# Optimization experiments

Measured on AMD Instinct MI355X. Metric: run time of the kernel, lower is better.

## Reference

```python
import jax, jax.numpy as jnp
import numpy as np

N = 50000      # nodes
E = 800000     # edges (before self loops)
F_IN = 128     # input feature dim
H = 4          # attention heads
C = 64         # per-head channels (hidden_dim = out_channels = 64)
HC = H * C     # 256, concat output width of each GATv2Conv
G = 32         # number of graphs in the batch
NEG_SLOPE_ATT = 0.2   # GATv2 internal LeakyReLU
NEG_SLOPE_ACT = 0.01  # encoder nn.LeakyReLU() default


def _glorot(key, shape, fan_in):
    return jax.random.normal(key, shape, jnp.float32) * (1.0 / np.sqrt(fan_in))


def setup_inputs() -> dict:
    key = jax.random.key(0)
    ks = jax.random.split(key, 32)
    inp = {}
    inp["x"] = jax.random.normal(ks[0], (N, F_IN), jnp.float32)
    inp["edge_index"] = jax.random.randint(ks[1], (2, E), 0, N, jnp.int32)
    inp["batch"] = jnp.sort(jax.random.randint(ks[2], (N,), 0, G, jnp.int32))
    i = 3
    for li, fin in ((1, F_IN), (2, HC), (3, HC)):
        inp[f"Wl{li}"] = _glorot(ks[i], (HC, fin), fin); i += 1
        inp[f"bl{li}"] = jnp.zeros((HC,), jnp.float32)
        inp[f"Wr{li}"] = _glorot(ks[i], (HC, fin), fin); i += 1
        inp[f"br{li}"] = jnp.zeros((HC,), jnp.float32)
        inp[f"att{li}"] = _glorot(ks[i], (H, C), C); i += 1
        inp[f"bo{li}"] = jnp.zeros((HC,), jnp.float32)
    return inp


def _gatv2_layer(x, src, dst, Wl, bl, Wr, br, att, bo):
    n = x.shape[0]
    xl = (x @ Wl.T + bl).reshape(n, H, C)  # source transform
    xr = (x @ Wr.T + br).reshape(n, H, C)  # target transform
    # per-edge attention logits: a^T LeakyReLU(xl[j] + xr[i])
    e = jax.nn.leaky_relu(xl[src] + xr[dst], negative_slope=NEG_SLOPE_ATT)  # [E', H, C]
    score = jnp.einsum('ehc,hc->eh', e, att)                                # [E', H]
    # segment softmax over incoming edges of each destination node
    m = jax.ops.segment_max(score, dst, num_segments=n)
    p = jnp.exp(score - m[dst])
    s = jax.ops.segment_sum(p, dst, num_segments=n)
    alpha = p / s[dst]
    out = jax.ops.segment_sum(alpha[:, :, None] * xl[src], dst, num_segments=n)
    return out.reshape(n, HC) + bo


def reference(x, edge_index, batch,
              Wl1, bl1, Wr1, br1, att1, bo1,
              Wl2, bl2, Wr2, br2, att2, bo2,
              Wl3, bl3, Wr3, br3, att3, bo3):
    loop = jnp.arange(N, dtype=edge_index.dtype)
    src = jnp.concatenate([edge_index[0], loop])  # add self loops (PyG default)
    dst = jnp.concatenate([edge_index[1], loop])
    h = _gatv2_layer(x, src, dst, Wl1, bl1, Wr1, br1, att1, bo1)
    h = jax.nn.leaky_relu(h, negative_slope=NEG_SLOPE_ACT)
    h = _gatv2_layer(h, src, dst, Wl2, bl2, Wr2, br2, att2, bo2)
    h = jax.nn.leaky_relu(h, negative_slope=NEG_SLOPE_ACT)
    h = _gatv2_layer(h, src, dst, Wl3, bl3, Wr3, br3, att3, bo3)
    # global mean pool over graphs
    sums = jax.ops.segment_sum(h, batch, num_segments=G)
    cnt = jax.ops.segment_sum(jnp.ones((N,), h.dtype), batch, num_segments=G)
    return sums / jnp.maximum(cnt, 1.0)[:, None]
```

## Files before the change

kernel.cpp:

```cpp
#include <hip/hip_runtime.h>

#define HEADS 4
#define CH 64
#define HC 256
#define NGRAPH 32
#define NEG_ATT 0.2f
#define NEG_ACT 0.01f

typedef __attribute__((ext_vector_type(8))) short bf16x8;
typedef __attribute__((ext_vector_type(4))) float f32x4;
typedef __attribute__((ext_vector_type(2))) float f32x2;

typedef __attribute__((address_space(3))) unsigned int lds_u32;
typedef const __attribute__((address_space(1))) unsigned int glob_u32;

__device__ __forceinline__ void gl_lds16(const void* g, void* l) {
  __builtin_amdgcn_global_load_lds((glob_u32*)(uintptr_t)g,
                                   (lds_u32*)(unsigned int)(uintptr_t)l, 16, 0, 0);
}

__device__ __forceinline__ void split2(float a, float b, unsigned& hi, unsigned& lo) {
  unsigned ua = __float_as_uint(a), ub = __float_as_uint(b);
  float la = a - __uint_as_float(ua & 0xFFFF0000u);
  float lb = b - __uint_as_float(ub & 0xFFFF0000u);
  hi = __builtin_amdgcn_perm(ub, ua, 0x07060302u);
  lo = __builtin_amdgcn_perm(__float_as_uint(lb), __float_as_uint(la), 0x07060302u);
}

__device__ __forceinline__ unsigned rtn_bf16(float f) {
  unsigned u = __float_as_uint(f);
  return (u + 0x7FFFu + ((u >> 16) & 1u)) >> 16;
}
__device__ __forceinline__ unsigned rtn_pack2(float a, float b) {
  return (rtn_bf16(b) << 16) | rtn_bf16(a);
}

__global__ __launch_bounds__(256) void convert_x(
    const float* __restrict__ X, unsigned short* __restrict__ xhi,
    unsigned short* __restrict__ xlo, int total4) {
  int g = blockIdx.x * 256 + threadIdx.x;
  if (g >= total4) return;
  float4 v = *(const float4*)&X[(size_t)g * 4];
  uint2 h2, l2;
  split2(v.x, v.y, h2.x, l2.x);
  split2(v.z, v.w, h2.y, l2.y);
  *(uint2*)&xhi[(size_t)g * 4] = h2;
  *(uint2*)&xlo[(size_t)g * 4] = l2;
}

__device__ __forceinline__ void conv_w_one(
    int g, const float* Wl, const float* Wr, int K,
    unsigned short* wfhi, unsigned short* wflo) {
  int lane = g & 63;
  int ct = (g >> 6) & 31;
  int kb = g >> 11;
  int col = ct * 16 + (lane & 15);
  int k = kb * 32 + (lane >> 4) * 8;
  const float* src = (col < HC) ? &Wl[(size_t)col * K + k] : &Wr[(size_t)(col - HC) * K + k];
  float4 v0 = *(const float4*)src;
  float4 v1 = *(const float4*)(src + 4);
  uint4 hq, lq;
  split2(v0.x, v0.y, hq.x, lq.x);
  split2(v0.z, v0.w, hq.y, lq.y);
  split2(v1.x, v1.y, hq.z, lq.z);
  split2(v1.z, v1.w, hq.w, lq.w);
  *(uint4*)&wfhi[(size_t)g * 8] = hq;
  *(uint4*)&wflo[(size_t)g * 8] = lq;
}

__global__ __launch_bounds__(256) void convert_w_all(
    const float* __restrict__ Wl1, const float* __restrict__ Wr1,
    unsigned short* __restrict__ w1hi, unsigned short* __restrict__ w1lo,
    const float* __restrict__ Wl2, const float* __restrict__ Wr2,
    unsigned short* __restrict__ w2hi, unsigned short* __restrict__ w2lo,
    const float* __restrict__ Wl3, const float* __restrict__ Wr3,
    unsigned short* __restrict__ w3hi, unsigned short* __restrict__ w3lo) {
  int g = blockIdx.x * 256 + threadIdx.x;
  if (g < 8192) conv_w_one(g, Wl1, Wr1, 128, w1hi, w1lo);
  else if (g < 8192 + 16384) conv_w_one(g - 8192, Wl2, Wr2, 256, w2hi, w2lo);
  else conv_w_one(g - 8192 - 16384, Wl3, Wr3, 256, w3hi, w3lo);
}

template <int K>
__global__ __launch_bounds__(256) void gemm_fused(
    const unsigned short* __restrict__ xhi, const unsigned short* __restrict__ xlo,
    const unsigned short* __restrict__ wfhi, const unsigned short* __restrict__ wflo,
    const float* __restrict__ bl, const float* __restrict__ br,
    unsigned short* __restrict__ Y1, unsigned short* __restrict__ Y2, int N, int nrb) {
  constexpr int nkb = K >> 5;
  __shared__ unsigned short Ah[2][128][32];
  __shared__ unsigned short Al[2][128][32];

  const int f = blockIdx.x;
  const int rb = (f & 7) + 8 * (f >> 5);
  const int cb = (f >> 3) & 3;
  if (rb >= nrb) return;

  const int tid = threadIdx.x;
  const int wave = tid >> 6;
  const int lane = tid & 63;
  const int quad = lane >> 4;
  const int l16 = lane & 15;
  const int wr = (wave >> 1) * 64;
  const int wc = (wave & 1) * 64;
  const int row0 = rb * 128;
  const int col0 = cb * 128;
  const int ctg0 = cb * 8 + (wave & 1) * 4;

  const int c0 = tid, c1 = tid + 256;
  const int r0g = row0 + (c0 >> 2), r1g = row0 + (c1 >> 2);
  const int ko0 = (c0 & 3) * 8, ko1 = (c1 & 3) * 8;
  const int gr0 = (r0g < N) ? r0g : N - 1;
  const int gr1 = (r1g < N) ? r1g : N - 1;

  f32x4 acc[4][4];
#pragma unroll
  for (int i = 0; i < 4; i++)
#pragma unroll
    for (int j = 0; j < 4; j++) acc[i][j] = (f32x4){0.f, 0.f, 0.f, 0.f};

  {
    size_t ga0 = (size_t)gr0 * K + ko0;
    size_t ga1 = (size_t)gr1 * K + ko1;
    gl_lds16(&xhi[ga0], &Ah[0][c0 >> 2][ko0]);
    gl_lds16(&xlo[ga0], &Al[0][c0 >> 2][ko0]);
    gl_lds16(&xhi[ga1], &Ah[0][c1 >> 2][ko1]);
    gl_lds16(&xlo[ga1], &Al[0][c1 >> 2][ko1]);
  }

#pragma unroll
  for (int kb = 0; kb < nkb; kb++) {
    const int cur = kb & 1, nxt = cur ^ 1;
    bf16x8 bhi[4], blo[4];
#pragma unroll
    for (int j = 0; j < 4; j++) {
      size_t ci = ((size_t)kb * 32 + ctg0 + j) * 64 + lane;
      bhi[j] = *(const bf16x8*)&wfhi[ci * 8];
      blo[j] = *(const bf16x8*)&wflo[ci * 8];
    }
    __syncthreads();
    if (kb + 1 < nkb) {
      int k0 = (kb + 1) * 32;
      size_t ga0 = (size_t)gr0 * K + k0 + ko0;
      size_t ga1 = (size_t)gr1 * K + k0 + ko1;
      gl_lds16(&xhi[ga0], &Ah[nxt][c0 >> 2][ko0]);
      gl_lds16(&xlo[ga0], &Al[nxt][c0 >> 2][ko0]);
      gl_lds16(&xhi[ga1], &Ah[nxt][c1 >> 2][ko1]);
      gl_lds16(&xlo[ga1], &Al[nxt][c1 >> 2][ko1]);
    }
    bf16x8 ahi[4], alo[4];
#pragma unroll
    for (int i = 0; i < 4; i++) {
      ahi[i] = *(const bf16x8*)&Ah[cur][wr + i * 16 + l16][quad * 8];
      alo[i] = *(const bf16x8*)&Al[cur][wr + i * 16 + l16][quad * 8];
    }
#pragma unroll
    for (int i = 0; i < 4; i++)
#pragma unroll
      for (int j = 0; j < 4; j++) {
        acc[i][j] = __builtin_amdgcn_mfma_f32_16x16x32_bf16(ahi[i], bhi[j], acc[i][j], 0, 0, 0);
        acc[i][j] = __builtin_amdgcn_mfma_f32_16x16x32_bf16(ahi[i], blo[j], acc[i][j], 0, 0, 0);
        acc[i][j] = __builtin_amdgcn_mfma_f32_16x16x32_bf16(alo[i], bhi[j], acc[i][j], 0, 0, 0);
      }
  }

#pragma unroll
  for (int j = 0; j < 4; j++) {
    int colg = col0 + wc + j * 16 + l16;
    unsigned short* Yp = (colg < HC) ? Y1 : Y2;
    int cc = (colg < HC) ? colg : colg - HC;
    float bv = (colg < HC) ? bl[cc] : br[cc];
#pragma unroll
    for (int i = 0; i < 4; i++)
#pragma unroll
      for (int r = 0; r < 4; r++) {
        int row = row0 + wr + i * 16 + quad * 4 + r;
        if (row < N)
          Yp[(size_t)row * HC + cc] = (unsigned short)rtn_bf16(acc[i][j][r] + bv);
      }
  }
}

__global__ __launch_bounds__(256) void hist_dst(
    const int* __restrict__ edst, int* __restrict__ counts, int E) {
  int e = blockIdx.x * 256 + threadIdx.x;
  if (e < E) atomicAdd(&counts[edst[e]], 1);
}

__global__ __launch_bounds__(256) void scan_blocks(
    const int* __restrict__ counts, int* __restrict__ row_start,
    int* __restrict__ bsum, int N) {
  __shared__ int tmp[256];
  int t = threadIdx.x;
  int base = blockIdx.x * 1024 + t * 4;
  int v0 = (base     < N) ? counts[base]     + 1 : 0;
  int v1 = (base + 1 < N) ? counts[base + 1] + 1 : 0;
  int v2 = (base + 2 < N) ? counts[base + 2] + 1 : 0;
  int v3 = (base + 3 < N) ? counts[base + 3] + 1 : 0;
  int c1 = v0 + v1, c2 = c1 + v2, tot = c2 + v3;
  tmp[t] = tot;
  __syncthreads();
  for (int off = 1; off < 256; off <<= 1) {
    int add = (t >= off) ? tmp[t - off] : 0;
    __syncthreads();
    tmp[t] += add;
    __syncthreads();
  }
  int excl = tmp[t] - tot;
  if (base     < N) row_start[base + 1] = excl + v0;
  if (base + 1 < N) row_start[base + 2] = excl + c1;
  if (base + 2 < N) row_start[base + 3] = excl + c2;
  if (base + 3 < N) row_start[base + 4] = excl + tot;
  if (t == 255) bsum[blockIdx.x] = tmp[255];
  if (blockIdx.x == 0 && t == 0) row_start[0] = 0;
}

__global__ void scan_tops(int* __restrict__ bsum, int nb) {
  int lane = threadIdx.x;
  int v = (lane < nb) ? bsum[lane] : 0;
  for (int off = 1; off < 64; off <<= 1) {
    int u = __shfl_up(v, off);
    if (lane >= off) v += u;
  }
  if (lane < nb) bsum[lane] = v;
}

__global__ __launch_bounds__(256) void scan_add(
    int* __restrict__ row_start, const int* __restrict__ bsum, int N) {
  int off = bsum[blockIdx.x];
  int i = (blockIdx.x + 1) * 1024 + threadIdx.x * 4;
#pragma unroll
  for (int k = 0; k < 4; k++)
    if (i + k < N) row_start[i + k + 1] += off;
}

__global__ __launch_bounds__(256) void csr_init(
    const int* __restrict__ row_start, int* __restrict__ fill_pos,
    int* __restrict__ csr_src, int N) {
  int i = blockIdx.x * 256 + threadIdx.x;
  if (i < N) {
    int p = row_start[i];
    csr_src[p] = i << 9;
    fill_pos[i] = p + 1;
  }
}

__global__ __launch_bounds__(256) void csr_scatter(
    const int* __restrict__ esrc, const int* __restrict__ edst,
    int* __restrict__ fill_pos, int* __restrict__ csr_src, int E) {
  int e = blockIdx.x * 256 + threadIdx.x;
  if (e < E) {
    int p = atomicAdd(&fill_pos[edst[e]], 1);
    csr_src[p] = esrc[e] << 9;
  }
}

__device__ __forceinline__ void unpk(uint2 q, f32x2& v01, f32x2& v23) {
  v01.x = __uint_as_float(q.x << 16);
  v01.y = __uint_as_float(q.x & 0xFFFF0000u);
  v23.x = __uint_as_float(q.y << 16);
  v23.y = __uint_as_float(q.y & 0xFFFF0000u);
}

__device__ __forceinline__ float edot(f32x2 l01, f32x2 l23, f32x2 r01, f32x2 r23,
                                      f32x2 a01, f32x2 a23) {
  f32x2 t01 = l01 + r01, t23 = l23 + r23;
  f32x2 u01 = t01 * NEG_ATT, u23 = t23 * NEG_ATT;
  t01.x = fmaxf(t01.x, u01.x); t01.y = fmaxf(t01.y, u01.y);
  t23.x = fmaxf(t23.x, u23.x); t23.y = fmaxf(t23.y, u23.y);
  f32x2 dv = t01 * a01 + t23 * a23;
  float d = dv.x + dv.y;
  d += __shfl_xor(d, 1);
  d += __shfl_xor(d, 2);
  d += __shfl_xor(d, 4);
  d += __shfl_xor(d, 8);
  return d;
}

__global__ __launch_bounds__(256) void gat_fused(
    const unsigned short* __restrict__ xl, const unsigned short* __restrict__ xr,
    const int* __restrict__ row_start, const int* __restrict__ csr_soff,
    const float* __restrict__ att, const float* __restrict__ bo,
    unsigned short* __restrict__ ohi, unsigned short* __restrict__ olo,
    int N, int mode) {
  int dst = (blockIdx.x * 256 + threadIdx.x) >> 6;
  int lane = threadIdx.x & 63;
  if (dst >= N) return;
  int h = lane >> 4;
  int off = h * CH + (lane & 15) * 4;
  const int loff = off * 2;
  const char* xlc = (const char*)xl;
  f32x2 a01 = *(const f32x2*)&att[off];
  f32x2 a23 = *(const f32x2*)&att[off + 2];
  f32x2 r01, r23;
  unpk(*(const uint2*)&xr[(size_t)dst * HC + off], r01, r23);
  f32x2 o01 = {0.f, 0.f}, o23 = {0.f, 0.f};
  float s = 0.f;
  int p = row_start[dst];
  int end = row_start[dst + 1];
  for (; p + 4 <= end; p += 4) {
    int b0 = csr_soff[p + 0] + loff, b1 = csr_soff[p + 1] + loff;
    int b2 = csr_soff[p + 2] + loff, b3 = csr_soff[p + 3] + loff;
    uint2 q0 = *(const uint2*)(xlc + b0);
    uint2 q1 = *(const uint2*)(xlc + b1);
    uint2 q2 = *(const uint2*)(xlc + b2);
    uint2 q3 = *(const uint2*)(xlc + b3);
    f32x2 l0a, l0b, l1a, l1b, l2a, l2b, l3a, l3b;
    unpk(q0, l0a, l0b);
    unpk(q1, l1a, l1b);
    unpk(q2, l2a, l2b);
    unpk(q3, l3a, l3b);
    float e0 = __expf(edot(l0a, l0b, r01, r23, a01, a23));
    float e1 = __expf(edot(l1a, l1b, r01, r23, a01, a23));
    float e2 = __expf(edot(l2a, l2b, r01, r23, a01, a23));
    float e3 = __expf(edot(l3a, l3b, r01, r23, a01, a23));
    s += (e0 + e1) + (e2 + e3);
    o01 = l0a * e0 + o01;
    o01 = l1a * e1 + o01;
    o01 = l2a * e2 + o01;
    o01 = l3a * e3 + o01;
    o23 = l0b * e0 + o23;
    o23 = l1b * e1 + o23;
    o23 = l2b * e2 + o23;
    o23 = l3b * e3 + o23;
  }
  for (; p < end; p++) {
    int b0 = csr_soff[p] + loff;
    uint2 q0 = *(const uint2*)(xlc + b0);
    f32x2 la, lb;
    unpk(q0, la, lb);
    float pe = __expf(edot(la, lb, r01, r23, a01, a23));
    s += pe;
    o01 = la * pe + o01;
    o23 = lb * pe + o23;
  }
  float inv = 1.f / s;
  f32x2 b01 = *(const f32x2*)&bo[off];
  f32x2 b23 = *(const f32x2*)&bo[off + 2];
  f32x2 res01 = o01 * inv + b01;
  f32x2 res23 = o23 * inv + b23;
  if (mode == 1) {
    f32x2 v01 = res01 * NEG_ACT, v23 = res23 * NEG_ACT;
    res01.x = fmaxf(res01.x, v01.x); res01.y = fmaxf(res01.y, v01.y);
    res23.x = fmaxf(res23.x, v23.x); res23.y = fmaxf(res23.y, v23.y);
    uint2 h2, l2;
    split2(res01.x, res01.y, h2.x, l2.x);
    split2(res23.x, res23.y, h2.y, l2.y);
    *(uint2*)&ohi[(size_t)dst * HC + off] = h2;
    *(uint2*)&olo[(size_t)dst * HC + off] = l2;
  } else {
    uint2 pk;
    pk.x = rtn_pack2(res01.x, res01.y);
    pk.y = rtn_pack2(res23.x, res23.y);
    *(uint2*)&ohi[(size_t)dst * HC + off] = pk;
  }
}

__global__ __launch_bounds__(256) void pool_direct(
    const unsigned short* __restrict__ h3, const int* __restrict__ batch,
    float* __restrict__ out, int N) {
  const int g = blockIdx.x;
  const int t = threadIdx.x;
  int lo = 0, hi = N;
  while (lo < hi) { int mid = (lo + hi) >> 1; if (batch[mid] < g) lo = mid + 1; else hi = mid; }
  int lo2 = lo, hi2 = N;
  while (lo2 < hi2) { int mid = (lo2 + hi2) >> 1; if (batch[mid] < g + 1) lo2 = mid + 1; else hi2 = mid; }
  const int cnt = lo2 - lo;
  const int colu = t & 127;
  const int rpar = t >> 7;
  f32x2 acc = {0.f, 0.f};
  const unsigned* h3u = (const unsigned*)h3;
  for (int n = lo + rpar; n < lo2; n += 2) {
    unsigned q = h3u[(size_t)n * 128 + colu];
    f32x2 v;
    v.x = __uint_as_float(q << 16);
    v.y = __uint_as_float(q & 0xFFFF0000u);
    acc += v;
  }
  __shared__ f32x2 sh[2][128];
  sh[rpar][colu] = acc;
  __syncthreads();
  if (t < 128) {
    f32x2 tot = sh[0][t] + sh[1][t];
    float c = (float)max(cnt, 1);
    f32x2 res = tot * (1.f / c);
    *(f32x2*)&out[g * HC + t * 2] = res;
  }
}

extern "C" void kernel_launch(void* const* d_in, const int* in_sizes, int n_in,
                              void* d_out, int out_size, void* d_ws, size_t ws_size,
                              hipStream_t stream) {
  const float* x = (const float*)d_in[0];
  const int* ei = (const int*)d_in[1];
  const int* batch = (const int*)d_in[2];
  const int N = in_sizes[2];
  const int E = in_sizes[1] / 2;
  const int Etot = E + N;

  const float* Wl[3] = {(const float*)d_in[3], (const float*)d_in[9], (const float*)d_in[15]};
  const float* bl[3] = {(const float*)d_in[4], (const float*)d_in[10], (const float*)d_in[16]};
  const float* Wr[3] = {(const float*)d_in[5], (const float*)d_in[11], (const float*)d_in[17]};
  const float* br[3] = {(const float*)d_in[6], (const float*)d_in[12], (const float*)d_in[18]};
  const float* att[3] = {(const float*)d_in[7], (const float*)d_in[13], (const float*)d_in[19]};
  const float* bo[3] = {(const float*)d_in[8], (const float*)d_in[14], (const float*)d_in[20]};

  float* B0 = (float*)d_ws;
  float* B1 = B0 + (size_t)N * HC;
  float* B2 = B1 + (size_t)N * HC;
  unsigned short* w1hi = (unsigned short*)(B2 + (size_t)N * HC);
  unsigned short* w1lo = w1hi + 512 * 128;
  unsigned short* w2hi = w1lo + 512 * 128;
  unsigned short* w2lo = w2hi + 512 * 256;
  unsigned short* w3hi = w2lo + 512 * 256;
  unsigned short* w3lo = w3hi + 512 * 256;
  int* counts = (int*)(w3lo + 512 * 256);
  int* row_start = counts + N;
  int* bsum = row_start + N + 1;
  int* fill_pos = bsum + 64;
  int* csr_src = fill_pos + N;

  unsigned short* xlB = (unsigned short*)B1;
  unsigned short* xrB = (unsigned short*)B2;
  unsigned short* xhiL1 = (unsigned short*)B0;
  unsigned short* xloL1 = xhiL1 + (size_t)N * 128;
  unsigned short* xhiL = (unsigned short*)B0;
  unsigned short* xloL = xhiL + (size_t)N * HC;
  unsigned short* h3B = (unsigned short*)B0;

  const int* esrc = ei;
  const int* edst = ei + E;

  convert_x<<<(N * 128 / 4 + 255) / 256, 256, 0, stream>>>(x, xhiL1, xloL1, N * 128 / 4);
  convert_w_all<<<(8192 + 16384 + 16384) / 256, 256, 0, stream>>>(
      Wl[0], Wr[0], w1hi, w1lo, Wl[1], Wr[1], w2hi, w2lo, Wl[2], Wr[2], w3hi, w3lo);

  const int nscan = (N + 1023) / 1024;
  (void)hipMemsetAsync(counts, 0, (size_t)N * sizeof(int), stream);
  hist_dst<<<(E + 255) / 256, 256, 0, stream>>>(edst, counts, E);
  scan_blocks<<<nscan, 256, 0, stream>>>(counts, row_start, bsum, N);
  scan_tops<<<1, 64, 0, stream>>>(bsum, nscan);
  scan_add<<<nscan - 1, 256, 0, stream>>>(row_start, bsum, N);
  csr_init<<<(N + 255) / 256, 256, 0, stream>>>(row_start, fill_pos, csr_src, N);
  csr_scatter<<<(E + 255) / 256, 256, 0, stream>>>(esrc, edst, fill_pos, csr_src, E);

  const int nrb = (N + 127) / 128;
  const int gblocks = ((nrb + 7) / 8) * 32;
  const int fblocks = (N * 64 + 255) / 256;

  gemm_fused<128><<<gblocks, 256, 0, stream>>>(xhiL1, xloL1, w1hi, w1lo, bl[0], br[0], xlB, xrB, N, nrb);
  gat_fused<<<fblocks, 256, 0, stream>>>(xlB, xrB, row_start, csr_src, att[0], bo[0],
                                         xhiL, xloL, N, 1);
  gemm_fused<256><<<gblocks, 256, 0, stream>>>(xhiL, xloL, w2hi, w2lo, bl[1], br[1], xlB, xrB, N, nrb);
  gat_fused<<<fblocks, 256, 0, stream>>>(xlB, xrB, row_start, csr_src, att[1], bo[1],
                                         xhiL, xloL, N, 1);
  gemm_fused<256><<<gblocks, 256, 0, stream>>>(xhiL, xloL, w3hi, w3lo, bl[2], br[2], xlB, xrB, N, nrb);
  gat_fused<<<fblocks, 256, 0, stream>>>(xlB, xrB, row_start, csr_src, att[2], bo[2],
                                         h3B, nullptr, N, 2);

  pool_direct<<<NGRAPH, 256, 0, stream>>>(h3B, batch, (float*)d_out, N);
}
```

Before: 800.7 us.

## Parallelize global mean pool across node chunks with LDS partials and atomics

Replaces the 32-block mean pool, which had one block per graph and a binary search over `batch`, with a two-kernel scheme. `pool_partial` runs one block per 256-node chunk and accumulates per-graph partial sums and node counts in shared memory. It then flushes only the nonzero partials to the output with global atomics, and `pool_final` divides by the counts. This spreads the bandwidth-bound read of the final bf16 feature matrix over far more blocks than the 32 graphs allowed. The cost is two added memsets, an extra launch, and nondeterministic float summation order.

Measured after the change: 648.0 us. 19.1% less time.

```diff
diff --git a/kernel.cpp b/kernel.cpp
--- a/kernel.cpp
+++ b/kernel.cpp
@@ -356,36 +356,42 @@
   }
 }
 
-__global__ __launch_bounds__(256) void pool_direct(
+__global__ __launch_bounds__(256) void pool_partial(
     const unsigned short* __restrict__ h3, const int* __restrict__ batch,
-    float* __restrict__ out, int N) {
-  const int g = blockIdx.x;
-  const int t = threadIdx.x;
-  int lo = 0, hi = N;
-  while (lo < hi) { int mid = (lo + hi) >> 1; if (batch[mid] < g) lo = mid + 1; else hi = mid; }
-  int lo2 = lo, hi2 = N;
-  while (lo2 < hi2) { int mid = (lo2 + hi2) >> 1; if (batch[mid] < g + 1) lo2 = mid + 1; else hi2 = mid; }
-  const int cnt = lo2 - lo;
-  const int colu = t & 127;
-  const int rpar = t >> 7;
-  f32x2 acc = {0.f, 0.f};
-  const unsigned* h3u = (const unsigned*)h3;
-  for (int n = lo + rpar; n < lo2; n += 2) {
-    unsigned q = h3u[(size_t)n * 128 + colu];
-    f32x2 v;
-    v.x = __uint_as_float(q << 16);
-    v.y = __uint_as_float(q & 0xFFFF0000u);
-    acc += v;
-  }
-  __shared__ f32x2 sh[2][128];
-  sh[rpar][colu] = acc;
+    float* __restrict__ out, int* __restrict__ cnt, int N) {
+  __shared__ float part[NGRAPH][HC];
+  __shared__ int bsh[256];
+  __shared__ int cpart[NGRAPH];
+  int j = threadIdx.x;
+#pragma unroll
+  for (int g = 0; g < NGRAPH; g++) part[g][j] = 0.f;
+  if (j < NGRAPH) cpart[j] = 0;
+  int n0 = blockIdx.x * 256;
+  int nend = min(n0 + 256, N);
+  int nj = n0 + j;
+  bsh[j] = (nj < N) ? batch[nj] : 0;
   __syncthreads();
-  if (t < 128) {
-    f32x2 tot = sh[0][t] + sh[1][t];
-    float c = (float)max(cnt, 1);
-    f32x2 res = tot * (1.f / c);
-    *(f32x2*)&out[g * HC + t * 2] = res;
-  }
+  if (nj < nend) atomicAdd(&cpart[bsh[j]], 1);
+  for (int n = n0; n < nend; n++) {
+    int g = bsh[n - n0];
+    unsigned q = h3[(size_t)n * HC + j];
+    part[g][j] += __uint_as_float(q << 16);
+  }
+  __syncthreads();
+#pragma unroll
+  for (int g = 0; g < NGRAPH; g++) {
+    float v = part[g][j];
+    if (v != 0.f) atomicAdd(&out[g * HC + j], v);
+  }
+  if (j < NGRAPH && cpart[j] > 0) atomicAdd(&cnt[j], cpart[j]);
+}
+
+__global__ __launch_bounds__(256) void pool_final(
+    float* __restrict__ out, const int* __restrict__ cnt) {
+  int g = blockIdx.x;
+  int j = threadIdx.x;
+  float c = (float)max(cnt[g], 1);
+  out[g * HC + j] /= c;
 }
 
 extern "C" void kernel_launch(void* const* d_in, const int* in_sizes, int n_in,
@@ -419,6 +425,7 @@
   int* bsum = row_start + N + 1;
   int* fill_pos = bsum + 64;
   int* csr_src = fill_pos + N;
+  int* cnt = csr_src + Etot;
 
   unsigned short* xlB = (unsigned short*)B1;
   unsigned short* xrB = (unsigned short*)B2;
@@ -458,5 +465,8 @@
   gat_fused<<<fblocks, 256, 0, stream>>>(xlB, xrB, row_start, csr_src, att[2], bo[2],
                                          h3B, nullptr, N, 2);
 
-  pool_direct<<<NGRAPH, 256, 0, stream>>>(h3B, batch, (float*)d_out, N);
-}
+  (void)hipMemsetAsync(d_out, 0, NGRAPH * HC * sizeof(float), stream);
+  (void)hipMemsetAsync(cnt, 0, NGRAPH * sizeof(int), stream);
+  pool_partial<<<(N + 255) / 256, 256, 0, stream>>>(h3B, batch, (float*)d_out, cnt, N);
+  pool_final<<<NGRAPH, 256, 0, stream>>>((float*)d_out, cnt);
+}
```
